# Kernel tuning notes

Measured on AMD Instinct MI355X. Metric: run time of the kernel, lower is better.

## Reference

```python
import jax, jax.numpy as jnp
import numpy as np

HORIZONTAL = 4
VERTICAL = 4


def _laplacian3(x):
    """kornia.filters.laplacian(x, kernel_size=3): 3x3 all-ones kernel with
    center -8, normalized by sum(|k|)=16, reflect padding, depthwise conv.
    x: [B, C, H, W] -> [B, C, H, W]."""
    C = x.shape[1]
    k = np.ones((3, 3), dtype=np.float32)
    k[1, 1] = -8.0
    k /= 16.0  # kornia normalized=True
    kern = jnp.asarray(k, dtype=x.dtype)[None, None].repeat(C, axis=0)  # [C,1,3,3]
    xp = jnp.pad(x, ((0, 0), (0, 0), (1, 1), (1, 1)), mode="reflect")
    return jax.lax.conv_general_dilated(
        xp, kern, window_strides=(1, 1), padding="VALID",
        dimension_numbers=("NCHW", "OIHW", "NCHW"), feature_group_count=C)


def setup_inputs() -> dict:
    key = jax.random.key(0)
    k1, k2 = jax.random.split(key)
    shape = (32, 3, 512, 512)
    return {
        "ground_truth_batch": jax.random.normal(k1, shape, dtype=jnp.float32),
        "segmented_print_batch": jax.random.normal(k2, shape, dtype=jnp.float32),
    }


def reference(ground_truth_batch, segmented_print_batch):
    gt_grad = _laplacian3(ground_truth_batch)
    sp_grad = _laplacian3(segmented_print_batch)
    diff = jnp.abs(gt_grad - sp_grad)  # L1, reduction='sum' per block
    B, C, H, W = diff.shape
    vb, hb = H // VERTICAL, W // HORIZONTAL
    # Original code does image.reshape([H, W, C]) (flat reinterpret), then
    # sums |diff| over [vb, hb, C] blocks of that view. Reproduce exactly:
    d = diff.reshape(B, H, W, C)
    blocks = d.reshape(B, VERTICAL, vb, HORIZONTAL, hb, C).sum(axis=(2, 4, 5))  # [B, V, Hz]
    # Per image, keep the max-loss block; total loss = sum over batch.
    return jnp.max(blocks, axis=(1, 2)).sum()
```

## Files before the change

kernel.cpp:

```cpp
#include <hip/hip_runtime.h>

#define HH 512
#define WW 512
#define CC 3
#define BANDS 16
#define BAND_ROWS 32
#define RPW 8


__global__ __launch_bounds__(256, 2) void lap_block_sum_kernel(
    const float* __restrict__ gt, const float* __restrict__ sp,
    float* __restrict__ partial)
{
    __shared__ float ldsr[8][WW];
    __shared__ float red[4][4];

    const int band = blockIdx.x, c = blockIdx.y, b = blockIdx.z;
    const int t = threadIdx.x;
    const int wv = t >> 6, lane = t & 63;

    const size_t plane = (size_t)(b * CC + c) * (size_t)(HH * WW);
    const float* __restrict__ gtp = gt + plane;
    const float* __restrict__ spp = sp + plane;

    const int h0   = band * BAND_ROWS + wv * RPW;
    const int colA = 4 * lane;
    const int colB = 256 + 4 * lane;

    float hA[4], hB[4];
    {
        int hs = (wv == 0) ? h0 - 1 : h0 + RPW;
        hs = hs < 0 ? 1 : (hs > HH - 1 ? HH - 2 : hs);
        if (wv == 0 || wv == 3) {
            const float* gr = gtp + (size_t)hs * WW;
            const float* sr = spp + (size_t)hs * WW;
            float4 ga = *(const float4*)(gr + colA);
            float4 gb = *(const float4*)(gr + colB);
            float4 sa = *(const float4*)(sr + colA);
            float4 sb = *(const float4*)(sr + colB);
            hA[0]=ga.x-sa.x; hA[1]=ga.y-sa.y; hA[2]=ga.z-sa.z; hA[3]=ga.w-sa.w;
            hB[0]=gb.x-sb.x; hB[1]=gb.y-sb.y; hB[2]=gb.z-sb.z; hB[3]=gb.w-sb.w;
        }
    }

    float dA[RPW][4], dB[RPW][4];
    #pragma unroll
    for (int r = 0; r < RPW; ++r) {
        const float* gr = gtp + (size_t)(h0 + r) * WW;
        const float* sr = spp + (size_t)(h0 + r) * WW;
        float4 ga = *(const float4*)(gr + colA);
        float4 gb = *(const float4*)(gr + colB);
        float4 sa = *(const float4*)(sr + colA);
        float4 sb = *(const float4*)(sr + colB);
        dA[r][0]=ga.x-sa.x; dA[r][1]=ga.y-sa.y; dA[r][2]=ga.z-sa.z; dA[r][3]=ga.w-sa.w;
        dB[r][0]=gb.x-sb.x; dB[r][1]=gb.y-sb.y; dB[r][2]=gb.z-sb.z; dB[r][3]=gb.w-sb.w;
    }

    *(float4*)&ldsr[2*wv  ][colA] = make_float4(dA[0][0],dA[0][1],dA[0][2],dA[0][3]);
    *(float4*)&ldsr[2*wv  ][colB] = make_float4(dB[0][0],dB[0][1],dB[0][2],dB[0][3]);
    *(float4*)&ldsr[2*wv+1][colA] = make_float4(dA[RPW-1][0],dA[RPW-1][1],dA[RPW-1][2],dA[RPW-1][3]);
    *(float4*)&ldsr[2*wv+1][colB] = make_float4(dB[RPW-1][0],dB[RPW-1][1],dB[RPW-1][2],dB[RPW-1][3]);
    __syncthreads();

    float pA[4], pB[4], nA[4], nB[4];
    if (wv == 0) {
        pA[0]=hA[0]; pA[1]=hA[1]; pA[2]=hA[2]; pA[3]=hA[3];
        pB[0]=hB[0]; pB[1]=hB[1]; pB[2]=hB[2]; pB[3]=hB[3];
    } else {
        float4 a = *(const float4*)&ldsr[2*wv-1][colA];
        float4 q = *(const float4*)&ldsr[2*wv-1][colB];
        pA[0]=a.x; pA[1]=a.y; pA[2]=a.z; pA[3]=a.w;
        pB[0]=q.x; pB[1]=q.y; pB[2]=q.z; pB[3]=q.w;
    }
    if (wv == 3) {
        nA[0]=hA[0]; nA[1]=hA[1]; nA[2]=hA[2]; nA[3]=hA[3];
        nB[0]=hB[0]; nB[1]=hB[1]; nB[2]=hB[2]; nB[3]=hB[3];
    } else {
        float4 a = *(const float4*)&ldsr[2*wv+2][colA];
        float4 q = *(const float4*)&ldsr[2*wv+2][colB];
        nA[0]=a.x; nA[1]=a.y; nA[2]=a.z; nA[3]=a.w;
        nB[0]=q.x; nB[1]=q.y; nB[2]=q.z; nB[3]=q.w;
    }

    const int hzA0 = colA/384, hzA1 = (512+colA)/384, hzA2 = (1024+colA)/384;
    const int hzB0 = colB/384, hzB1 = (512+colB)/384, hzB2 = (1024+colB)/384;
    const int lm1 = (lane + 63) & 63, lp1 = (lane + 1) & 63;

    float acc0=0.f, acc1=0.f, acc2=0.f, acc3=0.f;
    int m = (c * HH + h0) % 3;

#define ROWSTEP(TA,TB,RM,BA,BB) do {                                    \
    float csA0 = TA[0]+dA[RM][0]+BA[0];                                 \
    float csA1 = TA[1]+dA[RM][1]+BA[1];                                 \
    float csA2 = TA[2]+dA[RM][2]+BA[2];                                 \
    float csA3 = TA[3]+dA[RM][3]+BA[3];                                 \
    float csB0 = TB[0]+dB[RM][0]+BB[0];                                 \
    float csB1 = TB[1]+dB[RM][1]+BB[1];                                 \
    float csB2 = TB[2]+dB[RM][2]+BB[2];                                 \
    float csB3 = TB[3]+dB[RM][3]+BB[3];                                 \
    float sA3m = __shfl(csA3, lm1), sA0p = __shfl(csA0, lp1);           \
    float sB3m = __shfl(csB3, lm1), sB0p = __shfl(csB0, lp1);           \
    float xR = __shfl(csB0, 0),     xL = __shfl(csA3, 63);              \
    float lA = (lane==0)  ? csA1 : sA3m;   \
    float rA = (lane==63) ? xR   : sA0p;                   \
    float lB = (lane==0)  ? xL   : sB3m;                   \
    float rB = (lane==63) ? csB2 : sB0p;    \
    float sA = fabsf(lA  +csA0+csA1 - 9.f*dA[RM][0])                    \
             + fabsf(csA0+csA1+csA2 - 9.f*dA[RM][1])                    \
             + fabsf(csA1+csA2+csA3 - 9.f*dA[RM][2])                    \
             + fabsf(csA2+csA3+rA   - 9.f*dA[RM][3]);                   \
    float sB = fabsf(lB  +csB0+csB1 - 9.f*dB[RM][0])                    \
             + fabsf(csB0+csB1+csB2 - 9.f*dB[RM][1])                    \
             + fabsf(csB1+csB2+csB3 - 9.f*dB[RM][2])                    \
             + fabsf(csB2+csB3+rB   - 9.f*dB[RM][3]);                   \
    int hzA = (m==0)?hzA0:((m==1)?hzA1:hzA2);                           \
    int hzB = (m==0)?hzB0:((m==1)?hzB1:hzB2);                           \
    acc0 += ((hzA==0)?sA:0.f) + ((hzB==0)?sB:0.f);                      \
    acc1 += ((hzA==1)?sA:0.f) + ((hzB==1)?sB:0.f);                      \
    acc2 += ((hzA==2)?sA:0.f) + ((hzB==2)?sB:0.f);                      \
    acc3 += ((hzA==3)?sA:0.f) + ((hzB==3)?sB:0.f);                      \
    m = (m==2)?0:(m+1);                                                 \
} while(0)

    ROWSTEP(pA,    pB,    0, dA[1], dB[1]);
    ROWSTEP(dA[0], dB[0], 1, dA[2], dB[2]);
    ROWSTEP(dA[1], dB[1], 2, dA[3], dB[3]);
    ROWSTEP(dA[2], dB[2], 3, dA[4], dB[4]);
    ROWSTEP(dA[3], dB[3], 4, dA[5], dB[5]);
    ROWSTEP(dA[4], dB[4], 5, dA[6], dB[6]);
    ROWSTEP(dA[5], dB[5], 6, dA[7], dB[7]);
    ROWSTEP(dA[6], dB[6], 7, nA,    nB);
#undef ROWSTEP

    #pragma unroll
    for (int off = 32; off > 0; off >>= 1) {
        acc0 += __shfl_xor(acc0, off);
        acc1 += __shfl_xor(acc1, off);
        acc2 += __shfl_xor(acc2, off);
        acc3 += __shfl_xor(acc3, off);
    }
    if (lane == 0) {
        red[wv][0] = acc0 * 0.0625f; red[wv][1] = acc1 * 0.0625f;
        red[wv][2] = acc2 * 0.0625f; red[wv][3] = acc3 * 0.0625f;
    }
    __syncthreads();
    if (t < 4) {
        const int wg = band + BANDS * (c + CC * b);
        partial[wg * 4 + t] = red[0][t] + red[1][t] + red[2][t] + red[3][t];
    }
}

__global__ void finalize_kernel(const float* __restrict__ partial,
                                float* __restrict__ out, int B)
{
    __shared__ float bmax[32];
    const int t = threadIdx.x;
    const int b = t >> 4, v = (t >> 2) & 3, hz = t & 3;
    float s = 0.f;
    if (b < B) {
        #pragma unroll
        for (int c = 0; c < CC; ++c) {
            #pragma unroll
            for (int band = 0; band < BANDS; ++band) {
                if ((c * HH + band * BAND_ROWS) / 384 == v)
                    s += partial[(band + BANDS * (c + CC * b)) * 4 + hz];
            }
        }
    }
    #pragma unroll
    for (int off = 8; off > 0; off >>= 1)
        s = fmaxf(s, __shfl_xor(s, off));
    if ((t & 15) == 0) bmax[b] = (b < B) ? s : 0.f;
    __syncthreads();
    if (t < 64) {
        float x = (t < 32) ? bmax[t] : 0.f;
        #pragma unroll
        for (int off = 16; off > 0; off >>= 1)
            x += __shfl_down(x, off);
        if (t == 0) out[0] = x;
    }
}

extern "C" void kernel_launch(void* const* d_in, const int* in_sizes, int n_in,
                              void* d_out, int out_size, void* d_ws, size_t ws_size,
                              hipStream_t stream) {
    const float* gt = (const float*)d_in[0];
    const float* sp = (const float*)d_in[1];
    float* partial = (float*)d_ws;
    float* out = (float*)d_out;

    const int B = in_sizes[0] / (CC * HH * WW);

    dim3 grid(BANDS, CC, B);
    lap_block_sum_kernel<<<grid, 256, 0, stream>>>(gt, sp, partial);

    finalize_kernel<<<1, 512, 0, stream>>>(partial, out, B);
}
```

Before: 43.39 us.

## Fuse finalize into main kernel via atomics and last-block reduction

Removes the separate finalize kernel launch. Each workgroup atomically adds its per-horizontal-block sums into a per-image block table, and the last workgroup to arrive, detected through an atomic counter, computes the per-image max and the batch sum. A memset is added to zero the workspace each call, and launch bounds are raised to 4 blocks per SM to allow more occupancy. This trades one kernel launch for atomics, a memset, and tighter register limits.

```diff
diff --git a/kernel.cpp b/kernel.cpp
--- a/kernel.cpp
+++ b/kernel.cpp
@@ -8,12 +8,15 @@
 #define RPW 8
 
 
-__global__ __launch_bounds__(256, 2) void lap_block_sum_kernel(
+__global__ __launch_bounds__(256, 4) void lap_block_sum_kernel(
     const float* __restrict__ gt, const float* __restrict__ sp,
-    float* __restrict__ partial)
+    float* __restrict__ blocks, unsigned* __restrict__ counter,
+    float* __restrict__ out, int nWG, int B)
 {
     __shared__ float ldsr[8][WW];
     __shared__ float red[4][4];
+    __shared__ int lastFlag;
+    __shared__ float bmax[32];
 
     const int band = blockIdx.x, c = blockIdx.y, b = blockIdx.z;
     const int t = threadIdx.x;
@@ -144,33 +147,38 @@
         red[wv][2] = acc2 * 0.0625f; red[wv][3] = acc3 * 0.0625f;
     }
     __syncthreads();
+
+    const int v = (c * HH + band * BAND_ROWS) / 384;
     if (t < 4) {
-        const int wg = band + BANDS * (c + CC * b);
-        partial[wg * 4 + t] = red[0][t] + red[1][t] + red[2][t] + red[3][t];
-    }
-}
-
-__global__ void finalize_kernel(const float* __restrict__ partial,
-                                float* __restrict__ out, int B)
-{
-    __shared__ float bmax[32];
-    const int t = threadIdx.x;
-    const int b = t >> 4, v = (t >> 2) & 3, hz = t & 3;
-    float s = 0.f;
-    if (b < B) {
-        #pragma unroll
-        for (int c = 0; c < CC; ++c) {
-            #pragma unroll
-            for (int band = 0; band < BANDS; ++band) {
-                if ((c * HH + band * BAND_ROWS) / 384 == v)
-                    s += partial[(band + BANDS * (c + CC * b)) * 4 + hz];
-            }
-        }
-    }
+        float r = red[0][t] + red[1][t] + red[2][t] + red[3][t];
+        atomicAdd(&blocks[(b * 4 + v) * 4 + t], r);
+    }
+    __syncthreads();
+
+    if (t == 0) {
+        __threadfence();
+        unsigned old = __hip_atomic_fetch_add(counter, 1u, __ATOMIC_ACQ_REL,
+                                              __HIP_MEMORY_SCOPE_AGENT);
+        lastFlag = (old == (unsigned)(nWG - 1));
+    }
+    __syncthreads();
+    if (!lastFlag) return;
+
+    __threadfence();
+    float x0 = (t < B * 16) ? __hip_atomic_load(&blocks[t], __ATOMIC_RELAXED,
+                                                __HIP_MEMORY_SCOPE_AGENT) : 0.f;
+    float x1 = (t + 256 < B * 16) ? __hip_atomic_load(&blocks[t + 256], __ATOMIC_RELAXED,
+                                                __HIP_MEMORY_SCOPE_AGENT) : 0.f;
     #pragma unroll
-    for (int off = 8; off > 0; off >>= 1)
-        s = fmaxf(s, __shfl_xor(s, off));
-    if ((t & 15) == 0) bmax[b] = (b < B) ? s : 0.f;
+    for (int off = 8; off > 0; off >>= 1) {
+        x0 = fmaxf(x0, __shfl_xor(x0, off));
+        x1 = fmaxf(x1, __shfl_xor(x1, off));
+    }
+    if ((t & 15) == 0) {
+        int b0 = t >> 4, b1 = b0 + 16;
+        if (b0 < B) bmax[b0] = x0;
+        if (b1 < 32) bmax[b1] = (b1 < B) ? x1 : 0.f;
+    }
     __syncthreads();
     if (t < 64) {
         float x = (t < 32) ? bmax[t] : 0.f;
@@ -186,13 +194,15 @@
                               hipStream_t stream) {
     const float* gt = (const float*)d_in[0];
     const float* sp = (const float*)d_in[1];
-    float* partial = (float*)d_ws;
+    float* blocks = (float*)d_ws;
+    unsigned* counter = (unsigned*)((char*)d_ws + 2048);
     float* out = (float*)d_out;
 
     const int B = in_sizes[0] / (CC * HH * WW);
 
+    hipMemsetAsync(d_ws, 0, 2048 + sizeof(unsigned), stream);
+
     dim3 grid(BANDS, CC, B);
-    lap_block_sum_kernel<<<grid, 256, 0, stream>>>(gt, sp, partial);
-
-    finalize_kernel<<<1, 512, 0, stream>>>(partial, out, B);
+    const int nWG = BANDS * CC * B;
+    lap_block_sum_kernel<<<grid, 256, 0, stream>>>(gt, sp, blocks, counter, out, nWG, B);
 }
```

Measured after the change: 164.4 us. +278.9%, slower.
